# Optimization experiments

Measured on AMD Instinct MI355X. Metric: run time of the kernel, lower is better.

## Reference

```python
import jax, jax.numpy as jnp
import numpy as np
from jax import lax

B, L, DM, NL = 2, 1024, 768, 4
E = 2 * DM          # d_inner
N = 16              # d_state
K = 4               # d_conv
R = DM // 16        # dt_rank = 48


def setup_inputs() -> dict:
    key = jax.random.key(0)
    ks = jax.random.split(key, 16)
    s = 0.02
    x = jax.random.normal(ks[0], (B, L, DM), jnp.float32)
    boundary_prob = jax.random.uniform(ks[1], (B, L, 1), jnp.float32)
    in_proj_w = jax.random.normal(ks[2], (NL, 2 * E, DM), jnp.float32) * s
    conv_w = jax.random.normal(ks[3], (NL, E, K), jnp.float32) * 0.3
    conv_b = jax.random.normal(ks[4], (NL, E), jnp.float32) * 0.02
    x_proj_w = jax.random.normal(ks[5], (NL, R + 2 * N, E), jnp.float32) * s
    dt_proj_w = jax.random.normal(ks[6], (NL, E, R), jnp.float32) * (R ** -0.5)
    dt_proj_b = jax.random.uniform(ks[7], (NL, E), jnp.float32, -4.6, -3.0)
    A_log = jnp.log(jnp.broadcast_to(jnp.arange(1, N + 1, dtype=jnp.float32), (NL, E, N)))
    ssm_D = jnp.ones((NL, E), jnp.float32)
    out_proj_w = jax.random.normal(ks[8], (NL, DM, E), jnp.float32) * s
    ln_w = jnp.ones((NL, DM), jnp.float32)
    ln_b = jnp.zeros((NL, DM), jnp.float32)
    normf_w = jnp.ones((DM,), jnp.float32)
    normf_b = jnp.zeros((DM,), jnp.float32)
    ctrl_w1 = jax.random.normal(ks[9], (DM, DM + 1), jnp.float32) * s
    ctrl_b1 = jnp.zeros((DM,), jnp.float32)
    ctrl_w2 = jax.random.normal(ks[10], (DM, DM), jnp.float32) * s
    ctrl_b2 = jnp.zeros((DM,), jnp.float32)
    out_ln_w = jnp.ones((DM,), jnp.float32)
    out_ln_b = jnp.zeros((DM,), jnp.float32)
    return dict(x=x, boundary_prob=boundary_prob, in_proj_w=in_proj_w, conv_w=conv_w,
                conv_b=conv_b, x_proj_w=x_proj_w, dt_proj_w=dt_proj_w, dt_proj_b=dt_proj_b,
                A_log=A_log, ssm_D=ssm_D, out_proj_w=out_proj_w, ln_w=ln_w, ln_b=ln_b,
                normf_w=normf_w, normf_b=normf_b, ctrl_w1=ctrl_w1, ctrl_b1=ctrl_b1,
                ctrl_w2=ctrl_w2, ctrl_b2=ctrl_b2, out_ln_w=out_ln_w, out_ln_b=out_ln_b)


def _layernorm(h, w, b):
    m = h.mean(-1, keepdims=True)
    v = ((h - m) ** 2).mean(-1, keepdims=True)
    return (h - m) * lax.rsqrt(v + 1e-5) * w + b


def reference(x, boundary_prob, in_proj_w, conv_w, conv_b, x_proj_w, dt_proj_w, dt_proj_b,
              A_log, ssm_D, out_proj_w, ln_w, ln_b, normf_w, normf_b,
              ctrl_w1, ctrl_b1, ctrl_w2, ctrl_b2, out_ln_w, out_ln_b):
    bsz = x.shape[0]

    def mamba_layer(h, i):
        # in_proj (no bias): [B,L,DM] -> [B,L,2E]
        xz = jnp.einsum('bld,ed->ble', h, in_proj_w[i])
        xp, z = jnp.split(xz, 2, axis=-1)
        # causal depthwise conv1d (kernel K) + SiLU
        xc = xp.transpose(0, 2, 1)  # [B,E,L]
        xc = lax.conv_general_dilated(xc, conv_w[i][:, None, :], (1,), [(K - 1, 0)],
                                      feature_group_count=E,
                                      dimension_numbers=('NCH', 'OIH', 'NCH'))
        xc = jax.nn.silu(xc + conv_b[i][None, :, None]).transpose(0, 2, 1)  # [B,L,E]
        # x_proj -> dt, Bmat, Cmat
        dbl = jnp.einsum('ble,re->blr', xc, x_proj_w[i])
        dt, Bm, Cm = dbl[..., :R], dbl[..., R:R + N], dbl[..., R + N:]
        dt = jax.nn.softplus(jnp.einsum('blr,er->ble', dt, dt_proj_w[i]) + dt_proj_b[i])
        A = -jnp.exp(A_log[i])  # [E,N]

        def step(hstate, inp):
            xt, dtt, Bt, Ct = inp  # [B,E],[B,E],[B,N],[B,N]
            dA = jnp.exp(dtt[:, :, None] * A)                      # [B,E,N]
            hstate = dA * hstate + (dtt * xt)[:, :, None] * Bt[:, None, :]
            return hstate, jnp.einsum('ben,bn->be', hstate, Ct)

        h0 = jnp.zeros((bsz, E, N), x.dtype)
        _, ys = lax.scan(step, h0, (xc.swapaxes(0, 1), dt.swapaxes(0, 1),
                                    Bm.swapaxes(0, 1), Cm.swapaxes(0, 1)))
        y = ys.swapaxes(0, 1) + xc * ssm_D[i]
        y = y * jax.nn.silu(z)
        return jnp.einsum('ble,de->bld', y, out_proj_w[i])  # out_proj, no bias

    # Mamba Block stack: residual-in-fp32, pre-LayerNorm
    hs, residual = x, None
    for i in range(NL):
        residual = hs if residual is None else hs + residual
        hs = mamba_layer(_layernorm(residual, ln_w[i], ln_b[i]), i)
    residual = hs + residual
    mixed = _layernorm(residual, normf_w, normf_b)

    # boundary-controlled gate
    g_in = jnp.concatenate([x, boundary_prob], axis=-1)
    h1 = jax.nn.silu(g_in @ ctrl_w1.T + ctrl_b1)
    gate = jax.nn.sigmoid(h1 @ ctrl_w2.T + ctrl_b2)
    out = x + gate * (mixed - x)
    return _layernorm(out, out_ln_w, out_ln_b), gate
```

## Files before the change

kernel.cpp:

```cpp
#include <hip/hip_runtime.h>
#include <math.h>

static constexpr int B_  = 2;
static constexpr int L_  = 1024;
static constexpr int DM_ = 768;
static constexpr int NL_ = 4;
static constexpr int E_  = 2 * DM_;
static constexpr int N_  = 16;
static constexpr int K_  = 4;
static constexpr int R_  = DM_ / 16;
static constexpr int M_  = B_ * L_;
static constexpr int NC_ = 64;
static constexpr int T_  = L_ / NC_;
static constexpr int G_  = 16;
static constexpr int GS_ = NC_ / G_;
static constexpr int SK_ = 16;
static constexpr int KS_ = E_ / SK_;
static constexpr int OPK_ = 4;
static constexpr int NBE_ = N_ * B_ * E_;
static constexpr float LOG2E_ = 1.44269504088896340736f;

typedef __bf16 bf16x8 __attribute__((ext_vector_type(8)));
typedef __bf16 bf16x4 __attribute__((ext_vector_type(4)));
typedef short short8  __attribute__((ext_vector_type(8)));
typedef float f32x4   __attribute__((ext_vector_type(4)));

__device__ __forceinline__ short f2bf(float x) {
    __bf16 h = (__bf16)x;
    return __builtin_bit_cast(short, h);
}
__device__ __forceinline__ void st8(short* p, float4 x, float4 y) {
    short8 s;
    s[0] = f2bf(x.x); s[1] = f2bf(x.y); s[2] = f2bf(x.z); s[3] = f2bf(x.w);
    s[4] = f2bf(y.x); s[5] = f2bf(y.y); s[6] = f2bf(y.z); s[7] = f2bf(y.w);
    *(short8*)p = s;
}

__device__ __forceinline__ void gload16(const void* g, void* l) {
    __builtin_amdgcn_global_load_lds(
        (const __attribute__((address_space(1))) unsigned int*)g,
        (__attribute__((address_space(3))) unsigned int*)l,
        16, 0, 0);
}

template<int BN>
__global__ __launch_bounds__(256) void gemm_bf16(
    const __bf16* __restrict__ A, int lda,
    const __bf16* __restrict__ W, int ldw,
    void* __restrict__ Cout, int ldc, int Kd, int out_bf16,
    const float* __restrict__ bias, int act,
    const float* __restrict__ u, const float* __restrict__ v, int vstride,
    void* __restrict__ Cout2, int splitN)
{
    constexpr int BM = 128;
    constexpr int WN = BN / 2;
    constexpr int FM = 4;
    constexpr int FN = WN / 16;

    __shared__ __bf16 As[BM * 32];
    __shared__ __bf16 Bs[BN * 32];

    const int tid  = threadIdx.x;
    const int lane = tid & 63;
    const int wave = tid >> 6;
    const int wr = wave >> 1, wc = wave & 1;
    const int bm = blockIdx.y * BM;
    const int bn = blockIdx.x * BN;
    const int sk = blockIdx.z;

    A += (size_t)sk * Kd;
    W += (size_t)sk * Kd;
    const size_t cz = (size_t)sk * (size_t)gridDim.y * BM * ldc;

    const int sr = tid >> 2;
    const int sc = (tid & 3) << 3;
    const __bf16* ag0 = A + (size_t)(bm + sr) * lda + sc;
    const __bf16* ag1 = A + (size_t)(bm + 64 + sr) * lda + sc;
    const __bf16* wg0 = W + (size_t)(bn + sr) * ldw + sc;
    const __bf16* wg1 = W + (size_t)(bn + 64 + sr) * ldw + sc;

    __bf16* lA0 = As + wave * 512;
    __bf16* lA1 = As + 2048 + wave * 512;
    __bf16* lB0 = Bs + wave * 512;
    __bf16* lB1 = Bs + 2048 + wave * 512;

    f32x4 acc[FM][FN];
#pragma unroll
    for (int i = 0; i < FM; ++i)
#pragma unroll
        for (int j = 0; j < FN; ++j)
            acc[i][j] = (f32x4){0.f, 0.f, 0.f, 0.f};

    const __bf16* ard = As + (wr * 64 + (lane & 15)) * 32 + ((lane >> 4) << 3);
    const __bf16* brd = Bs + (wc * WN + (lane & 15)) * 32 + ((lane >> 4) << 3);

    const int NT = Kd / 32;
    for (int t = 0; t < NT; ++t) {
        const int k0 = t * 32;
        __syncthreads();
        gload16(ag0 + k0, lA0);
        gload16(ag1 + k0, lA1);
        gload16(wg0 + k0, lB0);
        if constexpr (BN == 128) gload16(wg1 + k0, lB1);
        __syncthreads();
        bf16x8 af[FM], bf[FN];
#pragma unroll
        for (int m = 0; m < FM; ++m)
            af[m] = *(const bf16x8*)(ard + m * 512);
#pragma unroll
        for (int n = 0; n < FN; ++n)
            bf[n] = *(const bf16x8*)(brd + n * 512);
#pragma unroll
        for (int m = 0; m < FM; ++m)
#pragma unroll
            for (int n = 0; n < FN; ++n)
                acc[m][n] = __builtin_amdgcn_mfma_f32_16x16x32_bf16(
                    af[m], bf[n], acc[m][n], 0, 0, 0);
    }

#pragma unroll
    for (int m = 0; m < FM; ++m) {
        const int row0 = bm + wr * 64 + m * 16 + ((lane >> 4) << 2);
#pragma unroll
        for (int n = 0; n < FN; ++n) {
            const int col = bn + wc * WN + n * 16 + (lane & 15);
            const float bia = bias ? bias[col] : 0.f;
            const float vv = u ? v[(size_t)col * vstride] : 0.f;
#pragma unroll
            for (int r = 0; r < 4; ++r) {
                float val = acc[m][n][r] + bia;
                if (Cout2) {
                    if (col < splitN) {
                        ((__bf16*)Cout)[(size_t)(row0 + r) * ldc + col] =
                            (__bf16)val;
                    } else {
                        float sv = val / (1.f + __expf(-val));
                        ((__bf16*)Cout2)[(size_t)(row0 + r) * ldc +
                                         (col - splitN)] = (__bf16)sv;
                    }
                    continue;
                }
                if (u) val += u[row0 + r] * vv;
                if (act == 1)      val = val / (1.f + __expf(-val));
                else if (act == 2) val = 1.f / (1.f + __expf(-val));
                else if (act == 3) val = (val > 20.f) ? val : log1pf(__expf(val));
                size_t off = cz + (size_t)(row0 + r) * ldc + col;
                if (out_bf16) ((__bf16*)Cout)[off] = (__bf16)val;
                else          ((float*)Cout)[off]  = val;
            }
        }
    }
}

__global__ __launch_bounds__(256) void cvt_bf16_kernel(
    const float* __restrict__ src, __bf16* __restrict__ dst, int n8)
{
    int i = blockIdx.x * 256 + threadIdx.x;
    if (i >= n8) return;
    const float4* s = (const float4*)src;
    st8((short*)(dst + (size_t)i * 8), s[2 * i], s[2 * i + 1]);
}

__global__ __launch_bounds__(256) void cvt_cw1_kernel(
    const float* __restrict__ src, __bf16* __restrict__ dst)
{
    int idx = blockIdx.x * 256 + threadIdx.x;
    if (idx >= DM_ * DM_) return;
    int r = idx / DM_, c = idx % DM_;
    dst[idx] = (__bf16)src[(size_t)r * (DM_ + 1) + c];
}

__global__ __launch_bounds__(256) void cvt_dpw_kernel(
    const float* __restrict__ src, __bf16* __restrict__ dst)
{
    int idx = blockIdx.x * 256 + threadIdx.x;
    if (idx >= NL_ * E_ * 64) return;
    int col = idx & 63;
    int row = idx >> 6;
    dst[idx] = (col < R_) ? (__bf16)src[(size_t)row * R_ + col] : (__bf16)0.f;
}

__global__ __launch_bounds__(256) void cvt_av_kernel(
    const float* __restrict__ alog, float* __restrict__ av)
{
    int idx = blockIdx.x * 256 + threadIdx.x;
    if (idx >= NL_ * E_ * N_) return;
    av[idx] = -__expf(alog[idx]) * LOG2E_;
}

__global__ __launch_bounds__(256) void xproj_mfma(
    const float* __restrict__ A, const float* __restrict__ W,
    float* __restrict__ part)
{
    constexpr int SA = 40;
    __shared__ short As[128 * SA];
    __shared__ short Ws[80 * SA];

    const int tid  = threadIdx.x;
    const int lane = tid & 63;
    const int wave = tid >> 6;
    const int sk = blockIdx.x;
    const int bm = blockIdx.y * 128;
    const int kbase = sk * KS_;

    const int ar = tid >> 1;
    const int ac = (tid & 1) << 4;
    const float* aptr = A + (size_t)(bm + ar) * E_ + kbase + ac;
    short* awr = &As[ar * SA + ac];

    const bool wact = tid < 160;
    const int wrow = tid >> 1;
    const float* wptr = W + (size_t)wrow * E_ + kbase + ac;
    short* wwr = &Ws[wrow * SA + ac];

    f32x4 acc[2][5];
#pragma unroll
    for (int i = 0; i < 2; ++i)
#pragma unroll
        for (int j = 0; j < 5; ++j)
            acc[i][j] = (f32x4){0.f, 0.f, 0.f, 0.f};

    const short* ard = &As[(wave * 32 + (lane & 15)) * SA + ((lane >> 4) << 3)];
    const short* brd = &Ws[(lane & 15) * SA + ((lane >> 4) << 3)];

    float4 aR[4], wR[4];
    auto loadT = [&](int k0) {
#pragma unroll
        for (int i = 0; i < 4; ++i)
            aR[i] = *(const float4*)(aptr + k0 + i * 4);
        if (wact) {
#pragma unroll
            for (int i = 0; i < 4; ++i)
                wR[i] = *(const float4*)(wptr + k0 + i * 4);
        }
    };

    constexpr int NT = KS_ / 32;
    loadT(0);
    for (int t = 0; t < NT; ++t) {
        __syncthreads();
        st8(awr, aR[0], aR[1]);
        st8(awr + 8, aR[2], aR[3]);
        if (wact) {
            st8(wwr, wR[0], wR[1]);
            st8(wwr + 8, wR[2], wR[3]);
        }
        __syncthreads();
        if (t + 1 < NT) loadT((t + 1) * 32);
        bf16x8 af[2], bf[5];
#pragma unroll
        for (int m = 0; m < 2; ++m)
            af[m] = *(const bf16x8*)(ard + m * 16 * SA);
#pragma unroll
        for (int n = 0; n < 5; ++n)
            bf[n] = *(const bf16x8*)(brd + n * 16 * SA);
#pragma unroll
        for (int m = 0; m < 2; ++m)
#pragma unroll
            for (int n = 0; n < 5; ++n)
                acc[m][n] = __builtin_amdgcn_mfma_f32_16x16x32_bf16(
                    af[m], bf[n], acc[m][n], 0, 0, 0);
    }

    float* pout = part + (size_t)sk * M_ * 80;
#pragma unroll
    for (int m = 0; m < 2; ++m) {
        const int row0 = bm + wave * 32 + m * 16 + ((lane >> 4) << 2);
#pragma unroll
        for (int n = 0; n < 5; ++n) {
            const int col = n * 16 + (lane & 15);
#pragma unroll
            for (int r = 0; r < 4; ++r)
                pout[(size_t)(row0 + r) * 80 + col] = acc[m][n][r];
        }
    }
}

__global__ __launch_bounds__(256) void xproj_reduce(
    const float* __restrict__ part, float* __restrict__ dbl,
    __bf16* __restrict__ dbl_bf)
{
    int idx = blockIdx.x * 256 + threadIdx.x;
    int m = idx / 80, col = idx % 80;
    float s = 0.f;
#pragma unroll
    for (int k = 0; k < SK_; ++k) s += part[(size_t)k * M_ * 80 + idx];
    dbl[idx] = s;
    if (col < R_)       dbl_bf[(size_t)m * 64 + col] = (__bf16)s;
    else if (col >= 64) dbl_bf[(size_t)m * 64 + (col - 16)] = (__bf16)0.f;
}

__device__ __forceinline__ float block_sum(float val, float* sm) {
#pragma unroll
    for (int o = 32; o > 0; o >>= 1) val += __shfl_down(val, o);
    int lane = threadIdx.x & 63, wid = threadIdx.x >> 6;
    __syncthreads();
    if (lane == 0) sm[wid] = val;
    __syncthreads();
    return sm[0] + sm[1] + sm[2] + sm[3];
}

__global__ __launch_bounds__(256) void add_ln_kernel(
    const float* __restrict__ src, int nparts,
    float* __restrict__ resid,
    const float* __restrict__ w, const float* __restrict__ b,
    float* __restrict__ outf, __bf16* __restrict__ outb, int do_add)
{
    constexpr int D = DM_;
    const size_t pstride = (size_t)M_ * DM_;
    const int row = blockIdx.x;
    const int tid = threadIdx.x;
    __shared__ float sm[4];
    const float* sp = src + (size_t)row * D;
    float* rp = resid + (size_t)row * D;

    float v[3];
    float s = 0.f;
#pragma unroll
    for (int j = 0; j < 3; ++j) {
        int d = j * 256 + tid;
        float vv = sp[d];
        for (int k = 1; k < nparts; ++k) vv += sp[(size_t)k * pstride + d];
        if (do_add) vv += rp[d];
        rp[d] = vv;
        v[j] = vv;
        s += vv;
    }
    float mean = block_sum(s, sm) * (1.f / D);
    float s2 = 0.f;
#pragma unroll
    for (int j = 0; j < 3; ++j) { float dlt = v[j] - mean; s2 += dlt * dlt; }
    float var = block_sum(s2, sm) * (1.f / D);
    float inv = rsqrtf(var + 1e-5f);
#pragma unroll
    for (int j = 0; j < 3; ++j) {
        int d = j * 256 + tid;
        float r = (v[j] - mean) * inv * w[d] + b[d];
        if (outf) outf[(size_t)row * D + d] = r;
        if (outb) outb[(size_t)row * D + d] = (__bf16)r;
    }
}

__device__ __forceinline__ float4 ld4bf(const __bf16* p) {
    bf16x4 v = *(const bf16x4*)p;
    return (float4){(float)v[0], (float)v[1], (float)v[2], (float)v[3]};
}

__global__ __launch_bounds__(256) void conv_silu_kernel(
    const __bf16* __restrict__ xp, const float* __restrict__ cw,
    const float* __restrict__ cb, float* __restrict__ xc)
{
    const int idx = blockIdx.x * 256 + threadIdx.x;
    if (idx >= M_ * E_ / 4) return;
    const int ec = (idx % (E_ / 4)) * 4;
    const int m  = idx / (E_ / 4);
    const int l  = m % L_;

    const float4 z4 = {0.f, 0.f, 0.f, 0.f};
    const __bf16* base = xp + (size_t)m * E_ + ec;
    float4 x0 = ld4bf(base);
    float4 x1 = (l >= 1) ? ld4bf(base - E_) : z4;
    float4 x2 = (l >= 2) ? ld4bf(base - 2 * E_) : z4;
    float4 x3 = (l >= 3) ? ld4bf(base - 3 * E_) : z4;
    const float4* wp = (const float4*)(cw + (size_t)ec * 4);
    float4 w0 = wp[0], w1 = wp[1], w2 = wp[2], w3 = wp[3];
    float4 bv = *(const float4*)(cb + ec);

    float4 o;
    o.x = bv.x + x3.x * w0.x + x2.x * w0.y + x1.x * w0.z + x0.x * w0.w;
    o.y = bv.y + x3.y * w1.x + x2.y * w1.y + x1.y * w1.z + x0.y * w1.w;
    o.z = bv.z + x3.z * w2.x + x2.z * w2.y + x1.z * w2.z + x0.z * w2.w;
    o.w = bv.w + x3.w * w3.x + x2.w * w3.y + x1.w * w3.z + x0.w * w3.w;
    o.x = o.x / (1.f + __expf(-o.x));
    o.y = o.y / (1.f + __expf(-o.y));
    o.z = o.z / (1.f + __expf(-o.z));
    o.w = o.w / (1.f + __expf(-o.w));
    *(float4*)(xc + (size_t)m * E_ + ec) = o;
}

__global__ __launch_bounds__(256) void scan_part1(
    const float* __restrict__ xc, const __bf16* __restrict__ dt,
    const float* __restrict__ dbl, const float* __restrict__ avl2,
    float* __restrict__ sumA, float* __restrict__ sumH)
{
    const int gid = blockIdx.x * 256 + threadIdx.x;
    const int c = gid % (B_ * E_);
    const int chunk = gid / (B_ * E_);
    const int b = c / E_;
    const int e = c % E_;

    float Av[N_];
    {
        const float4* Ap = (const float4*)(avl2 + e * N_);
        float4 A0 = Ap[0], A1 = Ap[1], A2 = Ap[2], A3 = Ap[3];
        float Ax[N_] = {A0.x, A0.y, A0.z, A0.w, A1.x, A1.y, A1.z, A1.w,
                        A2.x, A2.y, A2.z, A2.w, A3.x, A3.y, A3.z, A3.w};
#pragma unroll
        for (int n = 0; n < N_; ++n) Av[n] = Ax[n];
    }

    float h[N_];
#pragma unroll
    for (int n = 0; n < N_; ++n) h[n] = 0.f;
    float dts = 0.f;

    const size_t m0 = (size_t)b * L_ + (size_t)chunk * T_;
    for (int l = 0; l < T_; ++l) {
        size_t m = m0 + l;
        float dtv = (float)dt[m * E_ + e];
        float xv  = xc[m * E_ + e];
        float dtx = dtv * xv;
        const float4* Bp = (const float4*)(dbl + m * 80 + R_);
        float4 B0 = Bp[0], B1 = Bp[1], B2 = Bp[2], B3 = Bp[3];
        float Bv[N_] = {B0.x, B0.y, B0.z, B0.w, B1.x, B1.y, B1.z, B1.w,
                        B2.x, B2.y, B2.z, B2.w, B3.x, B3.y, B3.z, B3.w};
        dts += dtv;
#pragma unroll
        for (int n = 0; n < N_; ++n) {
            float dA = exp2f(dtv * Av[n]);
            h[n] = dA * h[n] + dtx * Bv[n];
        }
    }
#pragma unroll
    for (int n = 0; n < N_; ++n) {
        size_t o = (size_t)chunk * NBE_ + (size_t)n * (B_ * E_) + c;
        sumA[o] = exp2f(Av[n] * dts);
        sumH[o] = h[n];
    }
}

__global__ __launch_bounds__(256) void scan_part2a(
    const float* __restrict__ sumA, const float* __restrict__ sumH,
    float* __restrict__ gsumA, float* __restrict__ gsumH)
{
    const int gidx = blockIdx.x * 256 + threadIdx.x;
    const int g = gidx / NBE_;
    const int idx = gidx % NBE_;
    float a = 1.f, h = 0.f;
#pragma unroll
    for (int j = 0; j < GS_; ++j) {
        size_t o = (size_t)(g * GS_ + j) * NBE_ + idx;
        float aj = sumA[o];
        h = aj * h + sumH[o];
        a *= aj;
    }
    gsumA[(size_t)g * NBE_ + idx] = a;
    gsumH[(size_t)g * NBE_ + idx] = h;
}

__global__ __launch_bounds__(256) void scan_part2b(
    const float* __restrict__ gsumA, float* __restrict__ gsumH)
{
    const int idx = blockIdx.x * 256 + threadIdx.x;
    if (idx >= NBE_) return;
    float h = 0.f;
#pragma unroll
    for (int g = 0; g < G_; ++g) {
        size_t o = (size_t)g * NBE_ + idx;
        float a = gsumA[o];
        float hh = gsumH[o];
        gsumH[o] = h;
        h = a * h + hh;
    }
}

__global__ __launch_bounds__(256) void scan_part2c(
    const float* __restrict__ sumA, float* __restrict__ sumH,
    const float* __restrict__ gsumH)
{
    const int gidx = blockIdx.x * 256 + threadIdx.x;
    const int g = gidx / NBE_;
    const int idx = gidx % NBE_;
    float h = gsumH[(size_t)g * NBE_ + idx];
#pragma unroll
    for (int j = 0; j < GS_; ++j) {
        size_t o = (size_t)(g * GS_ + j) * NBE_ + idx;
        float a  = sumA[o];
        float hh = sumH[o];
        sumH[o] = h;
        h = a * h + hh;
    }
}

__global__ __launch_bounds__(256) void scan_part3(
    const float* __restrict__ xc, const __bf16* __restrict__ dt,
    const float* __restrict__ dbl, const __bf16* __restrict__ siluz,
    const float* __restrict__ avl2, const float* __restrict__ ssm_D,
    const float* __restrict__ hstart, __bf16* __restrict__ y)
{
    const int gid = blockIdx.x * 256 + threadIdx.x;
    const int c = gid % (B_ * E_);
    const int chunk = gid / (B_ * E_);
    const int b = c / E_;
    const int e = c % E_;

    float Av[N_];
    {
        const float4* Ap = (const float4*)(avl2 + e * N_);
        float4 A0 = Ap[0], A1 = Ap[1], A2 = Ap[2], A3 = Ap[3];
        float Ax[N_] = {A0.x, A0.y, A0.z, A0.w, A1.x, A1.y, A1.z, A1.w,
                        A2.x, A2.y, A2.z, A2.w, A3.x, A3.y, A3.z, A3.w};
#pragma unroll
        for (int n = 0; n < N_; ++n) Av[n] = Ax[n];
    }
    const float Dv = ssm_D[e];

    float h[N_];
#pragma unroll
    for (int n = 0; n < N_; ++n)
        h[n] = hstart[(size_t)chunk * NBE_ + (size_t)n * (B_ * E_) + c];

    const size_t m0 = (size_t)b * L_ + (size_t)chunk * T_;
    for (int l = 0; l < T_; ++l) {
        size_t m = m0 + l;
        float dtv = (float)dt[m * E_ + e];
        float xv  = xc[m * E_ + e];
        float dtx = dtv * xv;
        const float4* Bp = (const float4*)(dbl + m * 80 + R_);
        float4 B0 = Bp[0], B1 = Bp[1], B2 = Bp[2], B3 = Bp[3];
        float4 C0 = Bp[4], C1 = Bp[5], C2 = Bp[6], C3 = Bp[7];
        float Bv[N_] = {B0.x, B0.y, B0.z, B0.w, B1.x, B1.y, B1.z, B1.w,
                        B2.x, B2.y, B2.z, B2.w, B3.x, B3.y, B3.z, B3.w};
        float Cv[N_] = {C0.x, C0.y, C0.z, C0.w, C1.x, C1.y, C1.z, C1.w,
                        C2.x, C2.y, C2.z, C2.w, C3.x, C3.y, C3.z, C3.w};
        float p = 0.f;
#pragma unroll
        for (int n = 0; n < N_; ++n) {
            float dA = exp2f(dtv * Av[n]);
            h[n] = dA * h[n] + dtx * Bv[n];
            p += h[n] * Cv[n];
        }
        float sz = (float)siluz[m * E_ + e];
        y[m * E_ + e] = (__bf16)((p + xv * Dv) * sz);
    }
}

__global__ __launch_bounds__(256) void final_out_kernel(
    const float* __restrict__ x, const float* __restrict__ gate,
    const float* __restrict__ mixed, const float* __restrict__ w,
    const float* __restrict__ b, float* __restrict__ outp)
{
    constexpr int D = DM_;
    const int row = blockIdx.x;
    const int tid = threadIdx.x;
    __shared__ float sm[4];
    const float* xp = x + (size_t)row * D;
    const float* gp = gate + (size_t)row * D;
    const float* mp = mixed + (size_t)row * D;

    float v[3];
    float s = 0.f;
#pragma unroll
    for (int j = 0; j < 3; ++j) {
        int d = j * 256 + tid;
        float xv = xp[d];
        float o = xv + gp[d] * (mp[d] - xv);
        v[j] = o;
        s += o;
    }
    float mean = block_sum(s, sm) * (1.f / D);
    float s2 = 0.f;
#pragma unroll
    for (int j = 0; j < 3; ++j) { float dlt = v[j] - mean; s2 += dlt * dlt; }
    float var = block_sum(s2, sm) * (1.f / D);
    float inv = rsqrtf(var + 1e-5f);
    float* op = outp + (size_t)row * D;
#pragma unroll
    for (int j = 0; j < 3; ++j) {
        int d = j * 256 + tid;
        op[d] = (v[j] - mean) * inv * w[d] + b[d];
    }
}

extern "C" void kernel_launch(void* const* d_in, const int* in_sizes, int n_in,
                              void* d_out, int out_size, void* d_ws, size_t ws_size,
                              hipStream_t stream)
{
    const float* x    = (const float*)d_in[0];
    const float* bp   = (const float*)d_in[1];
    const float* inw  = (const float*)d_in[2];
    const float* cw   = (const float*)d_in[3];
    const float* cb   = (const float*)d_in[4];
    const float* xpw  = (const float*)d_in[5];
    const float* dpw  = (const float*)d_in[6];
    const float* dpb  = (const float*)d_in[7];
    const float* alog = (const float*)d_in[8];
    const float* sD   = (const float*)d_in[9];
    const float* opw  = (const float*)d_in[10];
    const float* lnw  = (const float*)d_in[11];
    const float* lnb  = (const float*)d_in[12];
    const float* nfw  = (const float*)d_in[13];
    const float* nfb  = (const float*)d_in[14];
    const float* cw1  = (const float*)d_in[15];
    const float* cb1  = (const float*)d_in[16];
    const float* cw2  = (const float*)d_in[17];
    const float* cb2  = (const float*)d_in[18];
    const float* olnw = (const float*)d_in[19];
    const float* olnb = (const float*)d_in[20];
    float* out = (float*)d_out;

    float* p = (float*)d_ws;
    float* resid  = p;  p += (size_t)M_ * DM_;
    float* xcb    = p;  p += (size_t)M_ * E_;
    float* dblb   = p;  p += (size_t)M_ * 80;
    float* mixedf = p;  p += (size_t)M_ * DM_;
    float* sumA   = p;  p += (size_t)NC_ * NBE_;
    float* sumHst = p;  p += (size_t)NC_ * NBE_;
    float* gsumA  = p;  p += (size_t)G_ * NBE_;
    float* gsumH  = p;  p += (size_t)G_ * NBE_;
    float* part01 = p;  p += (size_t)OPK_ * M_ * DM_;
    float* xpart  = p;  p += (size_t)SK_ * M_ * 80;
    float* avl2   = p;  p += (size_t)NL_ * E_ * N_;
    __bf16* xp_bf  = (__bf16*)p; p += (size_t)M_ * E_ / 2;
    __bf16* y_bf   = (__bf16*)p; p += (size_t)M_ * E_ / 2;
    __bf16* z_bf   = (__bf16*)p; p += (size_t)M_ * E_ / 2;
    __bf16* dt_bf  = (__bf16*)p; p += (size_t)M_ * E_ / 2;
    __bf16* hln_bf = (__bf16*)p; p += (size_t)M_ * DM_ / 2;
    __bf16* dbl_bf = (__bf16*)p; p += (size_t)M_ * 64 / 2;
    __bf16* inw_bf = (__bf16*)p; p += (size_t)NL_ * 2 * E_ * DM_ / 2;
    __bf16* opw_bf = (__bf16*)p; p += (size_t)NL_ * DM_ * E_ / 2;
    __bf16* dpw_bf = (__bf16*)p; p += (size_t)NL_ * E_ * 64 / 2;
    __bf16* cw1b   = (__bf16*)p; p += (size_t)DM_ * DM_ / 2;
    __bf16* cw2b   = (__bf16*)p; p += (size_t)DM_ * DM_ / 2;
    __bf16* x_bf   = (__bf16*)p; p += (size_t)M_ * DM_ / 2;
    __bf16* h1_bf  = (__bf16*)p; p += (size_t)M_ * DM_ / 2;
    float* gate   = out + (size_t)M_ * DM_;

    cvt_bf16_kernel<<<(NL_ * 2 * E_ * DM_ / 8) / 256, 256, 0, stream>>>(
        inw, inw_bf, NL_ * 2 * E_ * DM_ / 8);
    cvt_bf16_kernel<<<(NL_ * DM_ * E_ / 8) / 256, 256, 0, stream>>>(
        opw, opw_bf, NL_ * DM_ * E_ / 8);
    cvt_cw1_kernel<<<(DM_ * DM_) / 256, 256, 0, stream>>>(cw1, cw1b);
    cvt_bf16_kernel<<<(DM_ * DM_ / 8 + 255) / 256, 256, 0, stream>>>(
        cw2, cw2b, DM_ * DM_ / 8);
    cvt_bf16_kernel<<<(M_ * DM_ / 8) / 256, 256, 0, stream>>>(
        x, x_bf, M_ * DM_ / 8);
    cvt_dpw_kernel<<<(NL_ * E_ * 64) / 256, 256, 0, stream>>>(dpw, dpw_bf);
    cvt_av_kernel<<<(NL_ * E_ * N_) / 256, 256, 0, stream>>>(alog, avl2);

    for (int i = 0; i < NL_; ++i) {
        if (i == 0)
            add_ln_kernel<<<M_, 256, 0, stream>>>(x, 1, resid,
                lnw, lnb, nullptr, hln_bf, 0);
        else
            add_ln_kernel<<<M_, 256, 0, stream>>>(part01, OPK_, resid,
                lnw + i * DM_, lnb + i * DM_, nullptr, hln_bf, 1);
        gemm_bf16<64><<<dim3(2 * E_ / 64, M_ / 128, 1), 256, 0, stream>>>(
            hln_bf, DM_, inw_bf + (size_t)i * 2 * E_ * DM_, DM_, xp_bf, E_,
            DM_, 0, nullptr, 0, nullptr, nullptr, 0, z_bf, E_);
        conv_silu_kernel<<<(M_ * E_ / 4) / 256, 256, 0, stream>>>(
            xp_bf, cw + (size_t)i * E_ * K_, cb + (size_t)i * E_, xcb);
        xproj_mfma<<<dim3(SK_, M_ / 128), 256, 0, stream>>>(
            xcb, xpw + (size_t)i * 80 * E_, xpart);
        xproj_reduce<<<(M_ * 80) / 256, 256, 0, stream>>>(xpart, dblb, dbl_bf);
        gemm_bf16<64><<<dim3(E_ / 64, M_ / 128, 1), 256, 0, stream>>>(
            dbl_bf, 64, dpw_bf + (size_t)i * E_ * 64, 64, dt_bf, E_,
            64, 1, dpb + (size_t)i * E_, 3, nullptr, nullptr, 0, nullptr, 0);
        scan_part1<<<(NC_ * B_ * E_) / 256, 256, 0, stream>>>(
            xcb, dt_bf, dblb, avl2 + (size_t)i * E_ * N_, sumA, sumHst);
        scan_part2a<<<(G_ * NBE_) / 256, 256, 0, stream>>>(
            sumA, sumHst, gsumA, gsumH);
        scan_part2b<<<(NBE_) / 256, 256, 0, stream>>>(gsumA, gsumH);
        scan_part2c<<<(G_ * NBE_) / 256, 256, 0, stream>>>(
            sumA, sumHst, gsumH);
        scan_part3<<<(NC_ * B_ * E_) / 256, 256, 0, stream>>>(
            xcb, dt_bf, dblb, z_bf, avl2 + (size_t)i * E_ * N_,
            sD + (size_t)i * E_, sumHst, y_bf);
        gemm_bf16<64><<<dim3(DM_ / 64, M_ / 128, OPK_), 256, 0, stream>>>(
            y_bf, E_, opw_bf + (size_t)i * DM_ * E_, E_, part01, DM_,
            E_ / OPK_, 0, nullptr, 0, nullptr, nullptr, 0, nullptr, 0);
    }

    add_ln_kernel<<<M_, 256, 0, stream>>>(part01, OPK_, resid,
        nfw, nfb, mixedf, nullptr, 1);
    gemm_bf16<64><<<dim3(DM_ / 64, M_ / 128, 1), 256, 0, stream>>>(
        x_bf, DM_, cw1b, DM_, h1_bf, DM_, DM_, 1,
        cb1, 1, bp, cw1 + DM_, DM_ + 1, nullptr, 0);
    gemm_bf16<64><<<dim3(DM_ / 64, M_ / 128, 1), 256, 0, stream>>>(
        h1_bf, DM_, cw2b, DM_, gate, DM_, DM_, 0,
        cb2, 2, nullptr, nullptr, 0, nullptr, 0);
    final_out_kernel<<<M_, 256, 0, stream>>>(x, gate, mixedf, olnw, olnb, out);
}
```

Measured before the change: 707.9 us.

## Shrink GEMM tiles to 64x64 and merge the three-pass chunk scan into one kernel

The bf16 MFMA GEMM now uses fixed 64x64 block tiles with 2x2 fragments per wave, in place of 128xBN tiles. This doubles the block count for every projection GEMM, which helps fill the GPU's CUs on the small M=2048 problems, at the cost of less operand reuse per tile load. The hierarchical inter-chunk scan (group reduce, group scan, group propagate) is replaced by one kernel that walks all 64 chunks sequentially per state element, with loads batched four at a time. This removes two launches and the group-sum buffers, but leaves a longer serial dependency chain per thread and only 192 blocks.

```diff
diff --git a/kernel.cpp b/kernel.cpp
--- a/kernel.cpp
+++ b/kernel.cpp
@@ -12,8 +12,6 @@
 static constexpr int M_  = B_ * L_;
 static constexpr int NC_ = 64;
 static constexpr int T_  = L_ / NC_;
-static constexpr int G_  = 16;
-static constexpr int GS_ = NC_ / G_;
 static constexpr int SK_ = 16;
 static constexpr int KS_ = E_ / SK_;
 static constexpr int OPK_ = 4;
@@ -43,7 +41,6 @@
         16, 0, 0);
 }
 
-template<int BN>
 __global__ __launch_bounds__(256) void gemm_bf16(
     const __bf16* __restrict__ A, int lda,
     const __bf16* __restrict__ W, int ldw,
@@ -52,10 +49,11 @@
     const float* __restrict__ u, const float* __restrict__ v, int vstride,
     void* __restrict__ Cout2, int splitN)
 {
-    constexpr int BM = 128;
-    constexpr int WN = BN / 2;
-    constexpr int FM = 4;
-    constexpr int FN = WN / 16;
+    constexpr int BM = 64;
+    constexpr int BN = 64;
+    constexpr int WN = 32;
+    constexpr int FM = 2;
+    constexpr int FN = 2;
 
     __shared__ __bf16 As[BM * 32];
     __shared__ __bf16 Bs[BN * 32];
@@ -75,14 +73,10 @@
     const int sr = tid >> 2;
     const int sc = (tid & 3) << 3;
     const __bf16* ag0 = A + (size_t)(bm + sr) * lda + sc;
-    const __bf16* ag1 = A + (size_t)(bm + 64 + sr) * lda + sc;
     const __bf16* wg0 = W + (size_t)(bn + sr) * ldw + sc;
-    const __bf16* wg1 = W + (size_t)(bn + 64 + sr) * ldw + sc;
 
     __bf16* lA0 = As + wave * 512;
-    __bf16* lA1 = As + 2048 + wave * 512;
     __bf16* lB0 = Bs + wave * 512;
-    __bf16* lB1 = Bs + 2048 + wave * 512;
 
     f32x4 acc[FM][FN];
 #pragma unroll
@@ -91,17 +85,15 @@
         for (int j = 0; j < FN; ++j)
             acc[i][j] = (f32x4){0.f, 0.f, 0.f, 0.f};
 
-    const __bf16* ard = As + (wr * 64 + (lane & 15)) * 32 + ((lane >> 4) << 3);
-    const __bf16* brd = Bs + (wc * WN + (lane & 15)) * 32 + ((lane >> 4) << 3);
+    const __bf16* ard = As + (wr * 32 + (lane & 15)) * 32 + ((lane >> 4) << 3);
+    const __bf16* brd = Bs + (wc * 32 + (lane & 15)) * 32 + ((lane >> 4) << 3);
 
     const int NT = Kd / 32;
     for (int t = 0; t < NT; ++t) {
         const int k0 = t * 32;
         __syncthreads();
         gload16(ag0 + k0, lA0);
-        gload16(ag1 + k0, lA1);
         gload16(wg0 + k0, lB0);
-        if constexpr (BN == 128) gload16(wg1 + k0, lB1);
         __syncthreads();
         bf16x8 af[FM], bf[FN];
 #pragma unroll
@@ -120,7 +112,7 @@
 
 #pragma unroll
     for (int m = 0; m < FM; ++m) {
-        const int row0 = bm + wr * 64 + m * 16 + ((lane >> 4) << 2);
+        const int row0 = bm + wr * 32 + m * 16 + ((lane >> 4) << 2);
 #pragma unroll
         for (int n = 0; n < FN; ++n) {
             const int col = bn + wc * WN + n * 16 + (lane & 15);
@@ -429,56 +421,23 @@
     }
 }
 
-__global__ __launch_bounds__(256) void scan_part2a(
-    const float* __restrict__ sumA, const float* __restrict__ sumH,
-    float* __restrict__ gsumA, float* __restrict__ gsumH)
-{
-    const int gidx = blockIdx.x * 256 + threadIdx.x;
-    const int g = gidx / NBE_;
-    const int idx = gidx % NBE_;
-    float a = 1.f, h = 0.f;
-#pragma unroll
-    for (int j = 0; j < GS_; ++j) {
-        size_t o = (size_t)(g * GS_ + j) * NBE_ + idx;
-        float aj = sumA[o];
-        h = aj * h + sumH[o];
-        a *= aj;
-    }
-    gsumA[(size_t)g * NBE_ + idx] = a;
-    gsumH[(size_t)g * NBE_ + idx] = h;
-}
-
-__global__ __launch_bounds__(256) void scan_part2b(
-    const float* __restrict__ gsumA, float* __restrict__ gsumH)
+__global__ __launch_bounds__(256) void scan_part2(
+    const float* __restrict__ sumA, float* __restrict__ sumH)
 {
     const int idx = blockIdx.x * 256 + threadIdx.x;
     if (idx >= NBE_) return;
     float h = 0.f;
-#pragma unroll
-    for (int g = 0; g < G_; ++g) {
-        size_t o = (size_t)g * NBE_ + idx;
-        float a = gsumA[o];
-        float hh = gsumH[o];
-        gsumH[o] = h;
-        h = a * h + hh;
-    }
-}
-
-__global__ __launch_bounds__(256) void scan_part2c(
-    const float* __restrict__ sumA, float* __restrict__ sumH,
-    const float* __restrict__ gsumH)
-{
-    const int gidx = blockIdx.x * 256 + threadIdx.x;
-    const int g = gidx / NBE_;
-    const int idx = gidx % NBE_;
-    float h = gsumH[(size_t)g * NBE_ + idx];
-#pragma unroll
-    for (int j = 0; j < GS_; ++j) {
-        size_t o = (size_t)(g * GS_ + j) * NBE_ + idx;
-        float a  = sumA[o];
-        float hh = sumH[o];
-        sumH[o] = h;
-        h = a * h + hh;
+    for (int j = 0; j < NC_; j += 4) {
+        size_t o0 = (size_t)(j + 0) * NBE_ + idx;
+        size_t o1 = (size_t)(j + 1) * NBE_ + idx;
+        size_t o2 = (size_t)(j + 2) * NBE_ + idx;
+        size_t o3 = (size_t)(j + 3) * NBE_ + idx;
+        float a0 = sumA[o0], a1 = sumA[o1], a2 = sumA[o2], a3 = sumA[o3];
+        float h0 = sumH[o0], h1 = sumH[o1], h2 = sumH[o2], h3 = sumH[o3];
+        sumH[o0] = h;  h = a0 * h + h0;
+        sumH[o1] = h;  h = a1 * h + h1;
+        sumH[o2] = h;  h = a2 * h + h2;
+        sumH[o3] = h;  h = a3 * h + h3;
     }
 }
 
@@ -606,8 +565,6 @@
     float* mixedf = p;  p += (size_t)M_ * DM_;
     float* sumA   = p;  p += (size_t)NC_ * NBE_;
     float* sumHst = p;  p += (size_t)NC_ * NBE_;
-    float* gsumA  = p;  p += (size_t)G_ * NBE_;
-    float* gsumH  = p;  p += (size_t)G_ * NBE_;
     float* part01 = p;  p += (size_t)OPK_ * M_ * DM_;
     float* xpart  = p;  p += (size_t)SK_ * M_ * 80;
     float* avl2   = p;  p += (size_t)NL_ * E_ * N_;
@@ -645,7 +602,7 @@
         else
             add_ln_kernel<<<M_, 256, 0, stream>>>(part01, OPK_, resid,
                 lnw + i * DM_, lnb + i * DM_, nullptr, hln_bf, 1);
-        gemm_bf16<64><<<dim3(2 * E_ / 64, M_ / 128, 1), 256, 0, stream>>>(
+        gemm_bf16<<<dim3(2 * E_ / 64, M_ / 64, 1), 256, 0, stream>>>(
             hln_bf, DM_, inw_bf + (size_t)i * 2 * E_ * DM_, DM_, xp_bf, E_,
             DM_, 0, nullptr, 0, nullptr, nullptr, 0, z_bf, E_);
         conv_silu_kernel<<<(M_ * E_ / 4) / 256, 256, 0, stream>>>(
@@ -653,30 +610,26 @@
         xproj_mfma<<<dim3(SK_, M_ / 128), 256, 0, stream>>>(
             xcb, xpw + (size_t)i * 80 * E_, xpart);
         xproj_reduce<<<(M_ * 80) / 256, 256, 0, stream>>>(xpart, dblb, dbl_bf);
-        gemm_bf16<64><<<dim3(E_ / 64, M_ / 128, 1), 256, 0, stream>>>(
+        gemm_bf16<<<dim3(E_ / 64, M_ / 64, 1), 256, 0, stream>>>(
             dbl_bf, 64, dpw_bf + (size_t)i * E_ * 64, 64, dt_bf, E_,
             64, 1, dpb + (size_t)i * E_, 3, nullptr, nullptr, 0, nullptr, 0);
         scan_part1<<<(NC_ * B_ * E_) / 256, 256, 0, stream>>>(
             xcb, dt_bf, dblb, avl2 + (size_t)i * E_ * N_, sumA, sumHst);
-        scan_part2a<<<(G_ * NBE_) / 256, 256, 0, stream>>>(
-            sumA, sumHst, gsumA, gsumH);
-        scan_part2b<<<(NBE_) / 256, 256, 0, stream>>>(gsumA, gsumH);
-        scan_part2c<<<(G_ * NBE_) / 256, 256, 0, stream>>>(
-            sumA, sumHst, gsumH);
+        scan_part2<<<(NBE_) / 256, 256, 0, stream>>>(sumA, sumHst);
         scan_part3<<<(NC_ * B_ * E_) / 256, 256, 0, stream>>>(
             xcb, dt_bf, dblb, z_bf, avl2 + (size_t)i * E_ * N_,
             sD + (size_t)i * E_, sumHst, y_bf);
-        gemm_bf16<64><<<dim3(DM_ / 64, M_ / 128, OPK_), 256, 0, stream>>>(
+        gemm_bf16<<<dim3(DM_ / 64, M_ / 64, OPK_), 256, 0, stream>>>(
             y_bf, E_, opw_bf + (size_t)i * DM_ * E_, E_, part01, DM_,
             E_ / OPK_, 0, nullptr, 0, nullptr, nullptr, 0, nullptr, 0);
     }
 
     add_ln_kernel<<<M_, 256, 0, stream>>>(part01, OPK_, resid,
         nfw, nfb, mixedf, nullptr, 1);
-    gemm_bf16<64><<<dim3(DM_ / 64, M_ / 128, 1), 256, 0, stream>>>(
+    gemm_bf16<<<dim3(DM_ / 64, M_ / 64, 1), 256, 0, stream>>>(
         x_bf, DM_, cw1b, DM_, h1_bf, DM_, DM_, 1,
         cb1, 1, bp, cw1 + DM_, DM_ + 1, nullptr, 0);
-    gemm_bf16<64><<<dim3(DM_ / 64, M_ / 128, 1), 256, 0, stream>>>(
+    gemm_bf16<<<dim3(DM_ / 64, M_ / 64, 1), 256, 0, stream>>>(
         h1_bf, DM_, cw2b, DM_, gate, DM_, DM_, 0,
         cb2, 2, nullptr, nullptr, 0, nullptr, 0);
     final_out_kernel<<<M_, 256, 0, stream>>>(x, gate, mixedf, olnw, olnb, out);
```

Measured after the change: 659.6 us. 1.07x faster.
